# Kernel tuning notes

Hardware: AMD Instinct MI355X
Metric: run time of the kernel (lower is better)

Reference implementation:

```python
import jax, jax.numpy as jnp
import numpy as np

EPS = 1e-7  # keras backend.epsilon()
KSZ = 3
STRIDE = 1
NUM_CAPS = 32        # output capsule types
NUM_CAPS_IN = 32     # input capsule types
POSE = 4             # 4x4 pose matrices
ROUTINGS = 3


def _patches(t, k, s):
    # t: [B, H, W, C] -> [B, Ho, Wo, k*k, C], patch index order i*k+j (row-major),
    # matching the tf depthwise_conv2d tile-filter trick + transpose in the source.
    B, H, W, C = t.shape
    Ho = (H - k) // s + 1
    Wo = (W - k) // s + 1
    return jnp.stack(
        [t[:, i:i + Ho * s:s, j:j + Wo * s:s, :] for i in range(k) for j in range(k)],
        axis=3,
    )


def setup_inputs() -> dict:
    key = jax.random.key(0)
    k1, k2, k3, k4 = jax.random.split(key, 4)
    B, H, W = 2, 14, 14
    KKI = KSZ * KSZ * NUM_CAPS_IN  # 288
    x = jax.random.normal(k1, (B, H, W, NUM_CAPS_IN, POSE * POSE + 1), dtype=jnp.float32)
    Wt = jax.random.normal(k2, (KKI, NUM_CAPS, POSE, POSE), dtype=jnp.float32) * 0.05
    beta_v = jax.random.normal(k3, (1, 1, 1, 1, NUM_CAPS, 1), dtype=jnp.float32) * 0.1
    beta_a = jax.random.normal(k4, (1, 1, 1, 1, NUM_CAPS, 1), dtype=jnp.float32) * 0.1
    return {"x": x, "W": Wt, "beta_v": beta_v, "beta_a": beta_a}


def _em_routing(V, a_i, beta_v, beta_a):
    # V: [B,Ho,Wo,KKI,NC,PP], a_i: [B,Ho,Wo,KKI,1,1]
    KKI, NC = V.shape[3], V.shape[4]
    R = jnp.full((KKI, NC, 1), 1.0 / NC, dtype=V.dtype)
    M_j = a_j = None
    for it in range(ROUTINGS):
        inv_temp = 1.0 + (min(ROUTINGS, 3.0) - 1.0) * it / max(1.0, ROUTINGS - 1.0)
        # --- maximization ---
        Rw = R * a_i                                    # [B,Ho,Wo,KKI,NC,1]
        Rsum = jnp.sum(Rw, axis=-3, keepdims=True)      # [B,Ho,Wo,1,NC,1]
        M_jk = jnp.sum(Rw * V, axis=-3, keepdims=True) / Rsum   # [B,Ho,Wo,1,NC,PP]
        # NOTE: source uses R_ij_sum (not R_ij) inside the variance sum; keep faithful.
        stdv = jnp.sqrt(jnp.sum(Rsum * jnp.square(V - M_jk), axis=-3, keepdims=True) / Rsum)
        cost_h = (beta_v + jnp.log(stdv + EPS)) * Rsum
        cost = jnp.sum(cost_h, axis=-1, keepdims=True)          # [B,Ho,Wo,1,NC,1]
        c_mean = jnp.mean(cost, axis=-2, keepdims=True)
        c_stdv = jnp.sqrt(jnp.sum(jnp.square(cost - c_mean), axis=-2, keepdims=True) / NC)
        a_cost = beta_a + (c_mean - cost) / (c_stdv + EPS)
        a_jk = jax.nn.sigmoid(inv_temp * a_cost)                # [B,Ho,Wo,1,NC,1]
        a_j = jnp.squeeze(jnp.squeeze(a_jk, axis=-3), axis=-1)  # [B,Ho,Wo,NC]
        M_j = jnp.squeeze(M_jk, axis=-3)                        # [B,Ho,Wo,NC,PP]
        if it < ROUTINGS - 1:
            # --- estimation ---
            log_a = jnp.log(a_j[..., None, :, None] + EPS)      # [B,Ho,Wo,1,NC,1]
            log_p = (log_a
                     - jnp.sum(jnp.square(V - M_jk) / (2.0 * jnp.square(stdv)), axis=-1, keepdims=True)
                     - jnp.sum(jnp.log(stdv + EPS), axis=-1, keepdims=True))
            R = jax.nn.softmax(log_p, axis=-2)                  # softmax over NC axis
    return M_j, a_j


def reference(x, W, beta_v, beta_a):
    B, H, Wd, Cin, _ = x.shape
    PP = POSE * POSE
    M_i = x[..., :PP]          # [B,H,W,Cin,16]
    a_i = x[..., PP]           # [B,H,W,Cin]
    # depthwise-conv patch extraction (conv path)
    Mp = _patches(M_i.reshape(B, H, Wd, Cin * PP), KSZ, STRIDE)   # [B,Ho,Wo,9,Cin*16]
    B_, Ho, Wo = Mp.shape[0], Mp.shape[1], Mp.shape[2]
    KKI = KSZ * KSZ * Cin
    Mp = Mp.reshape(B, Ho, Wo, KKI, POSE, POSE)
    ap = _patches(a_i, KSZ, STRIDE).reshape(B, Ho, Wo, KKI)
    # spatial transform: vote matrices V_ij = M_i @ W_ij
    V = jnp.einsum('bhwipq,icqr->bhwicpr', Mp, W)                 # [B,Ho,Wo,KKI,NC,4,4]
    V = V.reshape(B, Ho, Wo, KKI, NUM_CAPS, PP)
    a_in = ap[..., None, None]                                    # [B,Ho,Wo,KKI,1,1]
    M_j, a_j = _em_routing(V, a_in, beta_v, beta_a)
    # assemble output: [B,Ho,Wo,NC,16] poses concat sigmoid activation
    out = jnp.concatenate([M_j, jax.nn.sigmoid(a_j)[..., None]], axis=-1)
    return out  # [B,Ho,Wo,NC,17]
```

## Files before the change

kernel.cpp:

```cpp
#include <hip/hip_runtime.h>
#include <math.h>


#define EPSF 1e-7f
#define KKI 288
#define NC 32
#define NTHREADS 512
#define NSUB 16
#define IPT 18

__global__ __launch_bounds__(NTHREADS)
void caps_em_kernel(const float* __restrict__ x, const float* __restrict__ Wg,
                    const float* __restrict__ beta_v, const float* __restrict__ beta_a,
                    float* __restrict__ out)
{
    __shared__ float MpL[KKI * 16];
    __shared__ float apL[KKI];
    __shared__ float T1L[NC * 16];
    __shared__ float S1L[NC * 16];
    __shared__ float S2L[NC * 16];
    __shared__ float RsumL[NC];
    __shared__ float ML[NC * 17];
    __shared__ float I2L[NC * 17];
    __shared__ float constL[NC];
    __shared__ float aoutL[NC];

    const int t = threadIdx.x;
    const int bid = blockIdx.x;
    const int b = bid / 144;
    const int rem = bid - b * 144;
    const int ho = rem / 12;
    const int wo = rem - ho * 12;

    const int c = t & 31;
    const int isub = t >> 5;

    for (int idx = t; idx < KKI * 17; idx += NTHREADS) {
        int i = idx / 17;
        int e = idx - i * 17;
        int p = i >> 5, cin = i & 31;
        int di = p / 3, dj = p - di * 3;
        float vx = x[(((b * 14 + (ho + di)) * 14 + (wo + dj)) * 32 + cin) * 17 + e];
        if (e < 16) MpL[i * 16 + e] = vx; else apL[i] = vx;
    }
    for (int idx = t; idx < NC * 16; idx += NTHREADS) { T1L[idx] = 0.f; S1L[idx] = 0.f; S2L[idx] = 0.f; }
    if (t < NC) RsumL[t] = 0.f;
    __syncthreads();

    auto stats = [&](float inv_temp) {
        if (t < NC) {
            int cc = t;
            float rsum = RsumL[cc];
            float inv_rsum = 1.f / rsum;
            float bv = beta_v[cc];
            float cost = 0.f, slog = 0.f;
            #pragma unroll
            for (int d = 0; d < 16; ++d) {
                float m = T1L[cc * 16 + d] * inv_rsum;
                float var = S2L[cc * 16 + d] - 2.f * m * S1L[cc * 16 + d] + 288.f * m * m;
                var = fmaxf(var, 0.f);
                float stdv = sqrtf(var);
                float lg = logf(stdv + EPSF);
                slog += lg;
                cost += bv + lg;
                ML[cc * 17 + d] = m;
                I2L[cc * 17 + d] = 0.5f / var;
            }
            cost *= rsum;
            float csum = cost;
            csum += __shfl_xor(csum, 16); csum += __shfl_xor(csum, 8);
            csum += __shfl_xor(csum, 4);  csum += __shfl_xor(csum, 2);
            csum += __shfl_xor(csum, 1);
            float c_mean = csum * 0.03125f;
            float diff = cost - c_mean;
            float dsq = diff * diff;
            dsq += __shfl_xor(dsq, 16); dsq += __shfl_xor(dsq, 8);
            dsq += __shfl_xor(dsq, 4);  dsq += __shfl_xor(dsq, 2);
            dsq += __shfl_xor(dsq, 1);
            float c_stdv = sqrtf(dsq * 0.03125f);
            float a_cost = beta_a[cc] + (c_mean - cost) / (c_stdv + EPSF);
            float a_j = 1.f / (1.f + expf(-inv_temp * a_cost));
            constL[cc] = logf(a_j + EPSF) - slog;
            aoutL[cc] = 1.f / (1.f + expf(-a_j));
        }
    };

    {
        float t1[16], s1[16], s2[16];
        #pragma unroll
        for (int d = 0; d < 16; ++d) { t1[d] = 0.f; s1[d] = 0.f; s2[d] = 0.f; }
        float rsum = 0.f;
        for (int j = 0; j < IPT; ++j) {
            int i = isub * IPT + j;
            float a_i = apL[i];
            const float4* w4 = (const float4*)(Wg + (size_t)(i * NC + c) * 16);
            float wa[16], ma[16];
            ((float4*)wa)[0] = w4[0]; ((float4*)wa)[1] = w4[1];
            ((float4*)wa)[2] = w4[2]; ((float4*)wa)[3] = w4[3];
            const float4* mp4 = (const float4*)(MpL + i * 16);
            ((float4*)ma)[0] = mp4[0]; ((float4*)ma)[1] = mp4[1];
            ((float4*)ma)[2] = mp4[2]; ((float4*)ma)[3] = mp4[3];
            float v[16];
            #pragma unroll
            for (int p = 0; p < 4; ++p)
                #pragma unroll
                for (int r = 0; r < 4; ++r) {
                    float acc = ma[p * 4 + 0] * wa[0 * 4 + r];
                    acc = fmaf(ma[p * 4 + 1], wa[1 * 4 + r], acc);
                    acc = fmaf(ma[p * 4 + 2], wa[2 * 4 + r], acc);
                    acc = fmaf(ma[p * 4 + 3], wa[3 * 4 + r], acc);
                    v[p * 4 + r] = acc;
                }
            float rw = a_i * 0.03125f;
            rsum += rw;
            #pragma unroll
            for (int d = 0; d < 16; ++d) {
                t1[d] = fmaf(rw, v[d], t1[d]);
                s1[d] += v[d];
                s2[d] = fmaf(v[d], v[d], s2[d]);
            }
        }
        rsum += __shfl_xor(rsum, 32);
        #pragma unroll
        for (int d = 0; d < 16; ++d) {
            t1[d] += __shfl_xor(t1[d], 32);
            s1[d] += __shfl_xor(s1[d], 32);
            s2[d] += __shfl_xor(s2[d], 32);
        }
        if ((t & 32) == 0) {
            atomicAdd(&RsumL[c], rsum);
            #pragma unroll
            for (int d = 0; d < 16; ++d) {
                atomicAdd(&T1L[c * 16 + d], t1[d]);
                atomicAdd(&S1L[c * 16 + d], s1[d]);
                atomicAdd(&S2L[c * 16 + d], s2[d]);
            }
        }
        __syncthreads();
        stats(1.0f);
        __syncthreads();
    }

    for (int it = 1; it < 3; ++it) {
        float Mreg[16], i2[16];
        #pragma unroll
        for (int d = 0; d < 16; ++d) { Mreg[d] = ML[c * 17 + d]; i2[d] = I2L[c * 17 + d]; }
        float Kc = constL[c];
        for (int idx = t; idx < NC * 16; idx += NTHREADS) T1L[idx] = 0.f;
        if (t < NC) RsumL[t] = 0.f;
        __syncthreads();

        float t1[16];
        #pragma unroll
        for (int d = 0; d < 16; ++d) t1[d] = 0.f;
        float rsum = 0.f;
        for (int j = 0; j < IPT; ++j) {
            int i = isub * IPT + j;
            float a_i = apL[i];
            const float4* w4 = (const float4*)(Wg + (size_t)(i * NC + c) * 16);
            float wa[16], ma[16];
            ((float4*)wa)[0] = w4[0]; ((float4*)wa)[1] = w4[1];
            ((float4*)wa)[2] = w4[2]; ((float4*)wa)[3] = w4[3];
            const float4* mp4 = (const float4*)(MpL + i * 16);
            ((float4*)ma)[0] = mp4[0]; ((float4*)ma)[1] = mp4[1];
            ((float4*)ma)[2] = mp4[2]; ((float4*)ma)[3] = mp4[3];
            float v[16];
            #pragma unroll
            for (int p = 0; p < 4; ++p)
                #pragma unroll
                for (int r = 0; r < 4; ++r) {
                    float acc = ma[p * 4 + 0] * wa[0 * 4 + r];
                    acc = fmaf(ma[p * 4 + 1], wa[1 * 4 + r], acc);
                    acc = fmaf(ma[p * 4 + 2], wa[2 * 4 + r], acc);
                    acc = fmaf(ma[p * 4 + 3], wa[3 * 4 + r], acc);
                    v[p * 4 + r] = acc;
                }
            float lp = Kc;
            #pragma unroll
            for (int d = 0; d < 16; ++d) {
                float df = v[d] - Mreg[d];
                lp = fmaf(-df * df, i2[d], lp);
            }
            float mx = lp;
            mx = fmaxf(mx, __shfl_xor(mx, 16)); mx = fmaxf(mx, __shfl_xor(mx, 8));
            mx = fmaxf(mx, __shfl_xor(mx, 4));  mx = fmaxf(mx, __shfl_xor(mx, 2));
            mx = fmaxf(mx, __shfl_xor(mx, 1));
            float ex = expf(lp - mx);
            float s = ex;
            s += __shfl_xor(s, 16); s += __shfl_xor(s, 8);
            s += __shfl_xor(s, 4);  s += __shfl_xor(s, 2);
            s += __shfl_xor(s, 1);
            float r = ex / s;
            float rw = r * a_i;
            rsum += rw;
            #pragma unroll
            for (int d = 0; d < 16; ++d) t1[d] = fmaf(rw, v[d], t1[d]);
        }
        rsum += __shfl_xor(rsum, 32);
        #pragma unroll
        for (int d = 0; d < 16; ++d) t1[d] += __shfl_xor(t1[d], 32);
        if ((t & 32) == 0) {
            atomicAdd(&RsumL[c], rsum);
            #pragma unroll
            for (int d = 0; d < 16; ++d) atomicAdd(&T1L[c * 16 + d], t1[d]);
        }
        __syncthreads();
        stats(1.0f + (float)it);
        __syncthreads();
    }

    for (int idx = t; idx < NC * 17; idx += NTHREADS) {
        int cc = idx / 17;
        int e = idx - cc * 17;
        float val = (e < 16) ? ML[cc * 17 + e] : aoutL[cc];
        out[(size_t)bid * (NC * 17) + idx] = val;
    }
}

extern "C" void kernel_launch(void* const* d_in, const int* in_sizes, int n_in,
                              void* d_out, int out_size, void* d_ws, size_t ws_size,
                              hipStream_t stream) {
    const float* x  = (const float*)d_in[0];
    const float* W  = (const float*)d_in[1];
    const float* bv = (const float*)d_in[2];
    const float* ba = (const float*)d_in[3];
    float* out = (float*)d_out;
    caps_em_kernel<<<288, NTHREADS, 0, stream>>>(x, W, bv, ba, out);
}
```

Before: 208.0 us.

## Double block threads, parallelize per-capsule stats across 512 threads, use fast reciprocals

Raises the block to 1024 threads so each thread handles 9 input capsules instead of 18, and fully unrolls the per-thread loops. The serial 16-dimension statistics loop run by 32 threads is split across 512 threads with shuffle reductions, using an extra barrier between the two phases. Divisions are replaced with hardware approximate reciprocals, and shared stat arrays are padded to stride 17 to reduce LDS bank conflicts. The risks are lower occupancy and register pressure at 1024 threads, plus slight precision loss from the approximate reciprocal.

```diff
diff --git a/kernel.cpp b/kernel.cpp
--- a/kernel.cpp
+++ b/kernel.cpp
@@ -5,9 +5,12 @@
 #define EPSF 1e-7f
 #define KKI 288
 #define NC 32
-#define NTHREADS 512
-#define NSUB 16
-#define IPT 18
+#define NTHREADS 1024
+#define NSUB 32
+#define IPT 9
+#define ST 17
+
+__device__ __forceinline__ float rcp_fast(float v) { return __builtin_amdgcn_rcpf(v); }
 
 __global__ __launch_bounds__(NTHREADS)
 void caps_em_kernel(const float* __restrict__ x, const float* __restrict__ Wg,
@@ -16,13 +19,15 @@
 {
     __shared__ float MpL[KKI * 16];
     __shared__ float apL[KKI];
-    __shared__ float T1L[NC * 16];
-    __shared__ float S1L[NC * 16];
-    __shared__ float S2L[NC * 16];
+    __shared__ float T1L[NC * ST];
+    __shared__ float S1L[NC * ST];
+    __shared__ float S2L[NC * ST];
+    __shared__ float ML[NC * ST];
+    __shared__ float I2L[NC * ST];
     __shared__ float RsumL[NC];
-    __shared__ float ML[NC * 17];
-    __shared__ float I2L[NC * 17];
     __shared__ float constL[NC];
+    __shared__ float slogL[NC];
+    __shared__ float costL[NC];
     __shared__ float aoutL[NC];
 
     const int t = threadIdx.x;
@@ -34,6 +39,7 @@
 
     const int c = t & 31;
     const int isub = t >> 5;
+    const int iBase = isub * IPT;
 
     for (int idx = t; idx < KKI * 17; idx += NTHREADS) {
         int i = idx / 17;
@@ -43,30 +49,34 @@
         float vx = x[(((b * 14 + (ho + di)) * 14 + (wo + dj)) * 32 + cin) * 17 + e];
         if (e < 16) MpL[i * 16 + e] = vx; else apL[i] = vx;
     }
-    for (int idx = t; idx < NC * 16; idx += NTHREADS) { T1L[idx] = 0.f; S1L[idx] = 0.f; S2L[idx] = 0.f; }
+    for (int idx = t; idx < NC * ST; idx += NTHREADS) { T1L[idx] = 0.f; S1L[idx] = 0.f; S2L[idx] = 0.f; }
     if (t < NC) RsumL[t] = 0.f;
     __syncthreads();
 
-    auto stats = [&](float inv_temp) {
-        if (t < NC) {
-            int cc = t;
+    auto statsA = [&]() {
+        if (t < 512) {
+            const int cc = t >> 4, d = t & 15;
             float rsum = RsumL[cc];
-            float inv_rsum = 1.f / rsum;
-            float bv = beta_v[cc];
-            float cost = 0.f, slog = 0.f;
-            #pragma unroll
-            for (int d = 0; d < 16; ++d) {
-                float m = T1L[cc * 16 + d] * inv_rsum;
-                float var = S2L[cc * 16 + d] - 2.f * m * S1L[cc * 16 + d] + 288.f * m * m;
-                var = fmaxf(var, 0.f);
-                float stdv = sqrtf(var);
-                float lg = logf(stdv + EPSF);
-                slog += lg;
-                cost += bv + lg;
-                ML[cc * 17 + d] = m;
-                I2L[cc * 17 + d] = 0.5f / var;
+            float inv_rsum = rcp_fast(rsum);
+            float m = T1L[cc * ST + d] * inv_rsum;
+            float var = S2L[cc * ST + d] - 2.f * m * S1L[cc * ST + d] + 288.f * m * m;
+            var = fmaxf(var, 0.f);
+            float stdv = sqrtf(var);
+            float lg = logf(stdv + EPSF);
+            ML[cc * ST + d] = m;
+            I2L[cc * ST + d] = 0.5f * rcp_fast(var);
+            float sl = lg;
+            sl += __shfl_xor(sl, 1); sl += __shfl_xor(sl, 2);
+            sl += __shfl_xor(sl, 4); sl += __shfl_xor(sl, 8);
+            if (d == 0) {
+                slogL[cc] = sl;
+                costL[cc] = rsum * (16.f * beta_v[cc] + sl);
             }
-            cost *= rsum;
+        }
+    };
+    auto statsB = [&](float inv_temp) {
+        if (t < 32) {
+            float cost = costL[t];
             float csum = cost;
             csum += __shfl_xor(csum, 16); csum += __shfl_xor(csum, 8);
             csum += __shfl_xor(csum, 4);  csum += __shfl_xor(csum, 2);
@@ -78,10 +88,10 @@
             dsq += __shfl_xor(dsq, 4);  dsq += __shfl_xor(dsq, 2);
             dsq += __shfl_xor(dsq, 1);
             float c_stdv = sqrtf(dsq * 0.03125f);
-            float a_cost = beta_a[cc] + (c_mean - cost) / (c_stdv + EPSF);
+            float a_cost = beta_a[t] + (c_mean - cost) * rcp_fast(c_stdv + EPSF);
             float a_j = 1.f / (1.f + expf(-inv_temp * a_cost));
-            constL[cc] = logf(a_j + EPSF) - slog;
-            aoutL[cc] = 1.f / (1.f + expf(-a_j));
+            constL[t] = logf(a_j + EPSF) - slogL[t];
+            aoutL[t] = 1.f / (1.f + expf(-a_j));
         }
     };
 
@@ -90,17 +100,19 @@
         #pragma unroll
         for (int d = 0; d < 16; ++d) { t1[d] = 0.f; s1[d] = 0.f; s2[d] = 0.f; }
         float rsum = 0.f;
+        #pragma unroll
         for (int j = 0; j < IPT; ++j) {
-            int i = isub * IPT + j;
-            float a_i = apL[i];
-            const float4* w4 = (const float4*)(Wg + (size_t)(i * NC + c) * 16);
+            const int i = iBase + j;
             float wa[16], ma[16];
+            const float4* w4 = (const float4*)(Wg + ((size_t)(i * NC + c) << 4));
             ((float4*)wa)[0] = w4[0]; ((float4*)wa)[1] = w4[1];
             ((float4*)wa)[2] = w4[2]; ((float4*)wa)[3] = w4[3];
             const float4* mp4 = (const float4*)(MpL + i * 16);
             ((float4*)ma)[0] = mp4[0]; ((float4*)ma)[1] = mp4[1];
             ((float4*)ma)[2] = mp4[2]; ((float4*)ma)[3] = mp4[3];
-            float v[16];
+            float a_i = apL[i];
+            float rw = a_i * 0.03125f;
+            rsum += rw;
             #pragma unroll
             for (int p = 0; p < 4; ++p)
                 #pragma unroll
@@ -109,16 +121,11 @@
                     acc = fmaf(ma[p * 4 + 1], wa[1 * 4 + r], acc);
                     acc = fmaf(ma[p * 4 + 2], wa[2 * 4 + r], acc);
                     acc = fmaf(ma[p * 4 + 3], wa[3 * 4 + r], acc);
-                    v[p * 4 + r] = acc;
+                    const int d = p * 4 + r;
+                    t1[d] = fmaf(rw, acc, t1[d]);
+                    s1[d] += acc;
+                    s2[d] = fmaf(acc, acc, s2[d]);
                 }
-            float rw = a_i * 0.03125f;
-            rsum += rw;
-            #pragma unroll
-            for (int d = 0; d < 16; ++d) {
-                t1[d] = fmaf(rw, v[d], t1[d]);
-                s1[d] += v[d];
-                s2[d] = fmaf(v[d], v[d], s2[d]);
-            }
         }
         rsum += __shfl_xor(rsum, 32);
         #pragma unroll
@@ -131,22 +138,24 @@
             atomicAdd(&RsumL[c], rsum);
             #pragma unroll
             for (int d = 0; d < 16; ++d) {
-                atomicAdd(&T1L[c * 16 + d], t1[d]);
-                atomicAdd(&S1L[c * 16 + d], s1[d]);
-                atomicAdd(&S2L[c * 16 + d], s2[d]);
+                atomicAdd(&T1L[c * ST + d], t1[d]);
+                atomicAdd(&S1L[c * ST + d], s1[d]);
+                atomicAdd(&S2L[c * ST + d], s2[d]);
             }
         }
         __syncthreads();
-        stats(1.0f);
+        statsA();
+        __syncthreads();
+        statsB(1.0f);
         __syncthreads();
     }
 
     for (int it = 1; it < 3; ++it) {
         float Mreg[16], i2[16];
         #pragma unroll
-        for (int d = 0; d < 16; ++d) { Mreg[d] = ML[c * 17 + d]; i2[d] = I2L[c * 17 + d]; }
+        for (int d = 0; d < 16; ++d) { Mreg[d] = ML[c * ST + d]; i2[d] = I2L[c * ST + d]; }
         float Kc = constL[c];
-        for (int idx = t; idx < NC * 16; idx += NTHREADS) T1L[idx] = 0.f;
+        for (int idx = t; idx < NC * ST; idx += NTHREADS) T1L[idx] = 0.f;
         if (t < NC) RsumL[t] = 0.f;
         __syncthreads();
 
@@ -154,16 +163,17 @@
         #pragma unroll
         for (int d = 0; d < 16; ++d) t1[d] = 0.f;
         float rsum = 0.f;
+        #pragma unroll
         for (int j = 0; j < IPT; ++j) {
-            int i = isub * IPT + j;
-            float a_i = apL[i];
-            const float4* w4 = (const float4*)(Wg + (size_t)(i * NC + c) * 16);
+            const int i = iBase + j;
             float wa[16], ma[16];
+            const float4* w4 = (const float4*)(Wg + ((size_t)(i * NC + c) << 4));
             ((float4*)wa)[0] = w4[0]; ((float4*)wa)[1] = w4[1];
             ((float4*)wa)[2] = w4[2]; ((float4*)wa)[3] = w4[3];
             const float4* mp4 = (const float4*)(MpL + i * 16);
             ((float4*)ma)[0] = mp4[0]; ((float4*)ma)[1] = mp4[1];
             ((float4*)ma)[2] = mp4[2]; ((float4*)ma)[3] = mp4[3];
+            float a_i = apL[i];
             float v[16];
             #pragma unroll
             for (int p = 0; p < 4; ++p)
@@ -190,7 +200,7 @@
             s += __shfl_xor(s, 16); s += __shfl_xor(s, 8);
             s += __shfl_xor(s, 4);  s += __shfl_xor(s, 2);
             s += __shfl_xor(s, 1);
-            float r = ex / s;
+            float r = ex * rcp_fast(s);
             float rw = r * a_i;
             rsum += rw;
             #pragma unroll
@@ -202,17 +212,19 @@
         if ((t & 32) == 0) {
             atomicAdd(&RsumL[c], rsum);
             #pragma unroll
-            for (int d = 0; d < 16; ++d) atomicAdd(&T1L[c * 16 + d], t1[d]);
-        }
-        __syncthreads();
-        stats(1.0f + (float)it);
+            for (int d = 0; d < 16; ++d) atomicAdd(&T1L[c * ST + d], t1[d]);
+        }
+        __syncthreads();
+        statsA();
+        __syncthreads();
+        statsB(1.0f + (float)it);
         __syncthreads();
     }
 
     for (int idx = t; idx < NC * 17; idx += NTHREADS) {
         int cc = idx / 17;
         int e = idx - cc * 17;
-        float val = (e < 16) ? ML[cc * 17 + e] : aoutL[cc];
+        float val = (e < 16) ? ML[idx] : aoutL[cc];
         out[(size_t)bid * (NC * 17) + idx] = val;
     }
 }
```

Result: slower. 330.0 us (+58.7%).
